# Optimization experiments

Measured on AMD Instinct MI355X. Metric: run time of the kernel, lower is better.

Reference implementation:

```python
import jax, jax.numpy as jnp
import numpy as np


def setup_inputs() -> dict:
    key = jax.random.key(0)
    k1, k2 = jax.random.split(key)
    B, D, H, W = 32, 256, 32, 32
    K = 1024
    z = jax.random.normal(k1, (B, D, H, W), dtype=jnp.float32)
    # torch init is uniform(-1/K, 1/K); randn scaled keeps same scale class
    embedding_weight = jax.random.uniform(k2, (K, D), dtype=jnp.float32,
                                          minval=-1.0 / K, maxval=1.0 / K)
    return {"z": z, "embedding_weight": embedding_weight}


def reference(z, embedding_weight):
    # z: [B, D, H, W] -> [B, H, W, D]
    z_nhwc = jnp.transpose(z, (0, 2, 3, 1))
    B, H, W, D = z_nhwc.shape
    z_flat = z_nhwc.reshape(-1, D)                      # [N, D]
    # squared distances: ||z||^2 + ||e||^2 - 2 z @ e^T   -> [N, K]
    d = (jnp.sum(z_flat ** 2, axis=1, keepdims=True)
         + jnp.sum(embedding_weight ** 2, axis=1)
         - 2.0 * z_flat @ embedding_weight.T)
    min_encoding_indices = jnp.argmin(d, axis=1)        # [N] int
    z_q = embedding_weight[min_encoding_indices].reshape(B, H, W, D)
    memodecode_loss = (jax.lax.stop_gradient(z_q) - z_nhwc) ** 2  # [B,H,W,D]
    z_q_out = jnp.transpose(z_q, (0, 3, 1, 2))          # [B, D, H, W]
    return (z_q_out, min_encoding_indices, memodecode_loss)
```

## Files before the change

### kernel.cpp

```cpp
#include <hip/hip_runtime.h>

#define DD 256
#define HWN 1024
#define NN 32768
#define KK 1024
#define MARGIN 1e-4f
#define FLAGBIT (1 << 30)

#define ZQ_OFF   0
#define IDX_OFF  8388608
#define LOSS_OFF 8421376

#define WS_NEED 38146112

typedef __attribute__((ext_vector_type(8))) _Float16 f16x8;
typedef __attribute__((ext_vector_type(4))) float f32x4;

__device__ __forceinline__ ushort f2h(float x) {
    _Float16 h = (_Float16)x;
    return *reinterpret_cast<ushort*>(&h);
}
__device__ __forceinline__ float h2f(ushort u) {
    _Float16 h = *reinterpret_cast<_Float16*>(&u);
    return (float)h;
}

__device__ __forceinline__ int swz(int r, int kgi) {
    return (r << 2) + (kgi ^ (r & 3) ^ ((r >> 2) & 3));
}

__global__ __launch_bounds__(64) void k_e2(const float* __restrict__ E,
                                           float* __restrict__ e2) {
    int k = (blockIdx.x << 6) + threadIdx.x;
    const float* row = E + (size_t)k * DD;
    float half_[2];
#pragma unroll
    for (int h = 0; h < 2; ++h) {
        const float* a = row + (h << 7);
        float r[8];
#pragma unroll
        for (int j = 0; j < 8; ++j) r[j] = __fmul_rn(a[j], a[j]);
        for (int i = 8; i < 128; i += 8) {
#pragma unroll
            for (int j = 0; j < 8; ++j) {
                float x = a[i + j];
                r[j] = __fadd_rn(r[j], __fmul_rn(x, x));
            }
        }
        half_[h] = __fadd_rn(__fadd_rn(__fadd_rn(r[0], r[1]), __fadd_rn(r[2], r[3])),
                             __fadd_rn(__fadd_rn(r[4], r[5]), __fadd_rn(r[6], r[7])));
    }
    e2[k] = __fadd_rn(half_[0], half_[1]);
}

__global__ __launch_bounds__(256) void k_prepZ2(const float* __restrict__ Z,
                                                ushort* __restrict__ Zh,
                                                float* __restrict__ z2) {
    __shared__ float zc[32][257];
    const int g = blockIdx.x;
    const int b = g >> 5;
    const int hw0 = (g & 31) << 5;
    const int th = threadIdx.x;
    const int n0 = (b << 10) + hw0;

#pragma unroll
    for (int j = 0; j < 32; ++j) {
        int li = (j << 8) + th;
        int d = li >> 5;
        int hl = li & 31;
        zc[hl][d] = Z[(size_t)((b << 8) + d) * HWN + hw0 + hl];
    }
    __syncthreads();

    {
        int r = th >> 3, c = th & 7;
        ushort hs[32];
#pragma unroll
        for (int i = 0; i < 32; ++i) hs[i] = f2h(zc[r][(c << 5) + i]);
        size_t addr = (size_t)(n0 + r) * DD + (c << 5);
#pragma unroll
        for (int q = 0; q < 4; ++q)
            *reinterpret_cast<f16x8*>(&Zh[addr + (q << 3)]) =
                *reinterpret_cast<f16x8*>(&hs[q << 3]);
    }

    {
        const int row = th >> 3, j = th & 7;
        const float* a = &zc[row][0];
        float x0 = a[j];
        float r0 = __fmul_rn(x0, x0);
        float x1 = a[128 + j];
        float r1 = __fmul_rn(x1, x1);
#pragma unroll
        for (int i = 8; i < 128; i += 8) {
            float y0 = a[i + j];
            r0 = __fadd_rn(r0, __fmul_rn(y0, y0));
            float y1 = a[128 + i + j];
            r1 = __fadd_rn(r1, __fmul_rn(y1, y1));
        }
#pragma unroll
        for (int m = 1; m <= 4; m <<= 1) {
            r0 = __fadd_rn(r0, __shfl_xor(r0, m));
            r1 = __fadd_rn(r1, __shfl_xor(r1, m));
        }
        if (j == 0) z2[n0 + row] = __fadd_rn(r0, r1);
    }
}

__global__ __launch_bounds__(256) void k_z2(const float* __restrict__ Z,
                                            float* __restrict__ z2) {
    int n = (blockIdx.x << 8) + threadIdx.x;
    int b = n >> 10, hw = n & 1023;
    const float* base = Z + (size_t)(b << 8) * HWN + hw;
    float half_[2];
#pragma unroll
    for (int h = 0; h < 2; ++h) {
        const float* a = base + (size_t)(h << 7) * HWN;
        float r[8];
#pragma unroll
        for (int j = 0; j < 8; ++j) {
            float x = a[(size_t)j * HWN];
            r[j] = __fmul_rn(x, x);
        }
        for (int i = 8; i < 128; i += 8) {
#pragma unroll
            for (int j = 0; j < 8; ++j) {
                float x = a[(size_t)(i + j) * HWN];
                r[j] = __fadd_rn(r[j], __fmul_rn(x, x));
            }
        }
        half_[h] = __fadd_rn(__fadd_rn(__fadd_rn(r[0], r[1]), __fadd_rn(r[2], r[3])),
                             __fadd_rn(__fadd_rn(r[4], r[5]), __fadd_rn(r[6], r[7])));
    }
    z2[n] = __fadd_rn(half_[0], half_[1]);
}

__global__ __launch_bounds__(256) void k_prepE(const float* __restrict__ E,
                                               ushort* __restrict__ Eh,
                                               int* __restrict__ flagCount) {
    if (blockIdx.x == 0 && threadIdx.x == 0) *flagCount = 0;
    int i4 = (blockIdx.x << 8) + threadIdx.x;
    float4 v = *reinterpret_cast<const float4*>(&E[(size_t)i4 << 2]);
    v.x *= 1024.f; v.y *= 1024.f; v.z *= 1024.f; v.w *= 1024.f;
    ushort4 h;
    h.x = f2h(v.x); h.y = f2h(v.y); h.z = f2h(v.z); h.w = f2h(v.w);
    *reinterpret_cast<ushort4*>(&Eh[(size_t)i4 << 2]) = h;
}

__device__ __forceinline__ void stage_kc(const ushort* __restrict__ Zh,
                                         const ushort* __restrict__ Eh,
                                         ushort* ldsbuf, int n0, int c0, int kc,
                                         int wid, int lane) {
#pragma unroll
    for (int is = 0; is < 4; ++is) {
        const int chunk = (wid << 2) + is;
        const int arr = chunk >> 3;
        const int cb8 = chunk & 7;
        const int s = (cb8 << 6) + lane;
        const int r = s >> 2;
        const int kgi = (s & 3) ^ (r & 3) ^ ((r >> 2) & 3);
        const ushort* g = (arr == 0) ? Zh + (size_t)(n0 + r) * DD
                                     : Eh + (size_t)(c0 + r) * DD;
        g += (kc << 5) + (kgi << 3);
        ushort* l = ldsbuf + arr * 4096 + (cb8 << 9);
        __builtin_amdgcn_global_load_lds(
            (const __attribute__((address_space(1))) void*)g,
            (__attribute__((address_space(3))) void*)l, 16, 0, 0);
    }
}

__global__ __launch_bounds__(256) void k_dist_mfma(const ushort* __restrict__ Zh,
                                                   const ushort* __restrict__ Eh,
                                                   const float* __restrict__ e2,
                                                   float* __restrict__ part) {
    __shared__ ushort lds[2][2][4096];
    float (*red)[2][3] = reinterpret_cast<float (*)[2][3]>(&lds[0][0][0]);

    const int B = blockIdx.x;
    const int xcd = B & 7;
    const int j = B >> 3;
    const int cb = j & 7;
    const int rb = (xcd << 5) + (j >> 3);
    const int n0 = rb << 7, c0 = cb << 7;
    const int th = threadIdx.x;
    const int wid = th >> 6, lane = th & 63;
    const int wr = wid >> 1, wc = wid & 1;
    const int fr = lane & 15, kgi = lane >> 4;

    f32x4 acc[4][4];
#pragma unroll
    for (int i = 0; i < 4; ++i)
#pragma unroll
        for (int jj = 0; jj < 4; ++jj) acc[i][jj] = (f32x4){0.f, 0.f, 0.f, 0.f};

    int zoff[4], eoff[4];
#pragma unroll
    for (int mi = 0; mi < 4; ++mi)
        zoff[mi] = swz((wr << 6) + (mi << 4) + fr, kgi) << 4;
#pragma unroll
    for (int ni = 0; ni < 4; ++ni)
        eoff[ni] = swz((wc << 6) + (ni << 4) + fr, kgi) << 4;

    stage_kc(Zh, Eh, &lds[0][0][0], n0, c0, 0, wid, lane);

    for (int kc = 0; kc < 8; ++kc) {
        __builtin_amdgcn_s_barrier();
        if (kc < 7) {
            stage_kc(Zh, Eh, &lds[(kc + 1) & 1][0][0], n0, c0, kc + 1, wid, lane);
            asm volatile("s_waitcnt vmcnt(4)" ::: "memory");
        } else {
            asm volatile("s_waitcnt vmcnt(0)" ::: "memory");
        }
        __builtin_amdgcn_s_barrier();

        const char* zb  = (const char*)&lds[kc & 1][0][0];
        const char* ebh = (const char*)&lds[kc & 1][1][0];
        f16x8 za[4], ea[4];
#pragma unroll
        for (int mi = 0; mi < 4; ++mi)
            za[mi] = *reinterpret_cast<const f16x8*>(zb + zoff[mi]);
#pragma unroll
        for (int ni = 0; ni < 4; ++ni)
            ea[ni] = *reinterpret_cast<const f16x8*>(ebh + eoff[ni]);
        __builtin_amdgcn_s_setprio(1);
#pragma unroll
        for (int mi = 0; mi < 4; ++mi)
#pragma unroll
            for (int ni = 0; ni < 4; ++ni)
                acc[mi][ni] = __builtin_amdgcn_mfma_f32_16x16x32_f16(za[mi], ea[ni], acc[mi][ni], 0, 0, 0);
        __builtin_amdgcn_s_setprio(0);
    }

    __syncthreads();

    float e2v[4];
#pragma unroll
    for (int ni = 0; ni < 4; ++ni) e2v[ni] = e2[c0 + (wc << 6) + (ni << 4) + fr];

#pragma unroll
    for (int mi = 0; mi < 4; ++mi) {
#pragma unroll
        for (int jj = 0; jj < 4; ++jj) {
            float m1 = __builtin_inff(), m2 = __builtin_inff(), bi = 3.4e38f;
#pragma unroll
            for (int ni = 0; ni < 4; ++ni) {
                float s = fmaf(-0x1p-9f, acc[mi][ni][jj], e2v[ni]);
                float c = (float)(c0 + (wc << 6) + (ni << 4) + fr);
                if (s < m1)      { m2 = m1; m1 = s; bi = c; }
                else if (s < m2) { m2 = s; }
            }
#pragma unroll
            for (int m = 1; m <= 8; m <<= 1) {
                float om1 = __shfl_xor(m1, m);
                float om2 = __shfl_xor(m2, m);
                float obi = __shfl_xor(bi, m);
                if (om1 < m1)       { m2 = fminf(m1, om2); m1 = om1; bi = obi; }
                else if (om1 == m1) { bi = fminf(bi, obi); m2 = m1; }
                else                { m2 = fminf(m2, om1); }
            }
            if (fr == 0) {
                int row = (wr << 6) + (mi << 4) + (kgi << 2) + jj;
                red[row][wc][0] = m1; red[row][wc][1] = m2; red[row][wc][2] = bi;
            }
        }
    }
    __syncthreads();
    if (th < 128) {
        float M1 = red[th][0][0], M2 = red[th][0][1], I = red[th][0][2];
        float v1 = red[th][1][0], v2 = red[th][1][1], vi = red[th][1][2];
        if (v1 < M1)       { M2 = fminf(M1, v2); M1 = v1; I = vi; }
        else if (v1 == M1) { I = fminf(I, vi); M2 = M1; }
        else               { M2 = fminf(M2, v1); }
        size_t p = ((size_t)(n0 + th) * 8 + cb) * 3;
        part[p] = M1; part[p + 1] = M2; part[p + 2] = I;
    }
}

__global__ __launch_bounds__(256) void k_combine(const float* __restrict__ part,
                                                 int* __restrict__ bestIdx,
                                                 int* __restrict__ flagList,
                                                 int* __restrict__ flagCount) {
    int n = (blockIdx.x << 8) + threadIdx.x;
    const float* p = part + (size_t)n * 24;
    float M1 = __builtin_inff(), M2 = __builtin_inff(), I = 3.4e38f;
    for (int c = 0; c < 8; ++c) {
        float v1 = p[c * 3], v2 = p[c * 3 + 1], vi = p[c * 3 + 2];
        if (v1 < M1)       { M2 = fminf(M1, v2); M1 = v1; I = vi; }
        else if (v1 == M1) { I = fminf(I, vi); M2 = M1; }
        else               { M2 = fminf(M2, v1); }
    }
    bestIdx[n] = (int)I;
    if (M2 - M1 < MARGIN) {
        int pos = atomicAdd(flagCount, 1);
        flagList[pos] = n;
    }
}

__global__ __launch_bounds__(256) void k_refine3(const float* __restrict__ Z,
                                                 const float* __restrict__ E,
                                                 const float* __restrict__ e2,
                                                 const float* __restrict__ z2,
                                                 int* __restrict__ bestIdx,
                                                 const int* __restrict__ flagList,
                                                 const int* __restrict__ flagCount) {
    __shared__ float zsh[DD];
    __shared__ float gbv[16];
    __shared__ int gbi[16];
    const int th = threadIdx.x;
    const int g = th >> 4;
    const int l = th & 15;
    const int cnt = *flagCount;

    for (int i = blockIdx.x; i < cnt; i += (int)gridDim.x) {
        const int n = flagList[i];
        const int b = n >> 10, hw = n & 1023;
        __syncthreads();
        if (th < DD) zsh[th] = Z[(size_t)((b << 8) + th) * HWN + hw];
        __syncthreads();
        float zr[16];
#pragma unroll
        for (int jq = 0; jq < 16; ++jq) zr[jq] = zsh[(l << 4) + jq];
        const float z2v = z2[n];
        float gbest = __builtin_inff();
        int bi = 0;

        for (int it = 0; it < 16; ++it) {
            double dots[4];
#pragma unroll
            for (int u = 0; u < 4; ++u) {
                const int c = (it << 6) + (u << 4) + g;
                const float* er = &E[(size_t)c * DD + (l << 4)];
                float4 a0 = *reinterpret_cast<const float4*>(er);
                float4 a1 = *reinterpret_cast<const float4*>(er + 4);
                float4 a2 = *reinterpret_cast<const float4*>(er + 8);
                float4 a3 = *reinterpret_cast<const float4*>(er + 12);
                double s0 = (double)a0.x * zr[0]  + (double)a0.y * zr[1]
                          + (double)a0.z * zr[2]  + (double)a0.w * zr[3];
                double s1 = (double)a1.x * zr[4]  + (double)a1.y * zr[5]
                          + (double)a1.z * zr[6]  + (double)a1.w * zr[7];
                double s2 = (double)a2.x * zr[8]  + (double)a2.y * zr[9]
                          + (double)a2.z * zr[10] + (double)a2.w * zr[11];
                double s3 = (double)a3.x * zr[12] + (double)a3.y * zr[13]
                          + (double)a3.z * zr[14] + (double)a3.w * zr[15];
                dots[u] = (s0 + s1) + (s2 + s3);
            }
#pragma unroll
            for (int m = 1; m <= 8; m <<= 1) {
#pragma unroll
                for (int u = 0; u < 4; ++u)
                    dots[u] += __shfl_xor(dots[u], m);
            }
            if (l == 0) {
#pragma unroll
                for (int u = 0; u < 4; ++u) {
                    const int c = (it << 6) + (u << 4) + g;
                    float cc = (float)dots[u];
                    float t2 = __fmul_rn(2.0f, cc);
                    float gg = __fsub_rn(__fadd_rn(z2v, e2[c]), t2);
                    if (gg < gbest) { gbest = gg; bi = c; }
                }
            }
        }
        if (l == 0) { gbv[g] = gbest; gbi[g] = bi; }
        __syncthreads();
        if (th == 0) {
            float best = gbv[0]; int bbi = gbi[0];
            for (int q = 1; q < 16; ++q) {
                float v = gbv[q]; int vi = gbi[q];
                if (v < best || (v == best && vi < bbi)) { best = v; bbi = vi; }
            }
            bestIdx[n] = bbi;
        }
    }
}

#define UPD(m1, m2, i1, s, k)                            \
    do {                                                 \
        if ((s) < (m1)) { m2 = m1; m1 = (s); i1 = (k); } \
        else if ((s) < (m2)) { m2 = (s); }               \
    } while (0)

#define FMAJ(j, EV, C)                                   \
    acc[0][j] = fmaf(z4.x, EV.C, acc[0][j]);             \
    acc[1][j] = fmaf(z4.y, EV.C, acc[1][j]);             \
    acc[2][j] = fmaf(z4.z, EV.C, acc[2][j]);             \
    acc[3][j] = fmaf(z4.w, EV.C, acc[3][j]);

#define UROUND(u, C)                                                          \
    {                                                                         \
        float4 z4 = *reinterpret_cast<const float4*>(&zs[dq + u][ty4]);       \
        FMAJ(0, e0, C) FMAJ(1, e1, C) FMAJ(2, e2v, C) FMAJ(3, e3, C)          \
        FMAJ(4, e4, C) FMAJ(5, e5, C) FMAJ(6, e6, C) FMAJ(7, e7, C)           \
    }

__global__ __launch_bounds__(256, 3) void k_dist_f32(const float* __restrict__ Z,
                                                     const float* __restrict__ E,
                                                     const float* __restrict__ e2,
                                                     int* __restrict__ bestIdx) {
    __shared__ float zs[64][68];
    __shared__ float es[128][68];
    const int th = threadIdx.x;
    const int n0 = blockIdx.x << 6;
    const int b = n0 >> 10;
    const int hw0 = n0 & 1023;
    const int tx = th & 15;
    const int ty = th >> 4;
    const int ty4 = ty << 2;
    float m1[4], m2[4];
    int idx[4];
#pragma unroll
    for (int i = 0; i < 4; ++i) { m1[i] = __builtin_inff(); m2[i] = __builtin_inff(); idx[i] = 0; }
    for (int ct = 0; ct < 8; ++ct) {
        float acc[4][8];
#pragma unroll
        for (int i = 0; i < 4; ++i)
#pragma unroll
            for (int j = 0; j < 8; ++j) acc[i][j] = 0.f;
        for (int dc = 0; dc < 4; ++dc) {
            __syncthreads();
#pragma unroll
            for (int j = 0; j < 4; ++j) {
                int i4 = (j << 8) + th;
                int dd = i4 >> 4;
                int rr = (i4 & 15) << 2;
                *reinterpret_cast<float4*>(&zs[dd][rr]) =
                    *reinterpret_cast<const float4*>(
                        &Z[(size_t)((b << 8) + (dc << 6) + dd) * HWN + hw0 + rr]);
            }
#pragma unroll
            for (int j = 0; j < 8; ++j) {
                int i4 = (j << 8) + th;
                int c = i4 >> 4;
                int d4 = (i4 & 15) << 2;
                *reinterpret_cast<float4*>(&es[c][d4]) =
                    *reinterpret_cast<const float4*>(
                        &E[(size_t)((ct << 7) + c) * DD + (dc << 6) + d4]);
            }
            __syncthreads();
#pragma unroll
            for (int dq = 0; dq < 64; dq += 4) {
                float4 e0 = *reinterpret_cast<const float4*>(&es[tx][dq]);
                float4 e1 = *reinterpret_cast<const float4*>(&es[tx + 16][dq]);
                float4 e2v = *reinterpret_cast<const float4*>(&es[tx + 32][dq]);
                float4 e3 = *reinterpret_cast<const float4*>(&es[tx + 48][dq]);
                float4 e4 = *reinterpret_cast<const float4*>(&es[tx + 64][dq]);
                float4 e5 = *reinterpret_cast<const float4*>(&es[tx + 80][dq]);
                float4 e6 = *reinterpret_cast<const float4*>(&es[tx + 96][dq]);
                float4 e7 = *reinterpret_cast<const float4*>(&es[tx + 112][dq]);
                UROUND(0, x)
                UROUND(1, y)
                UROUND(2, z)
                UROUND(3, w)
            }
        }
#pragma unroll
        for (int j = 0; j < 8; ++j) {
            int c = (ct << 7) + tx + (j << 4);
            float en = e2[c];
#pragma unroll
            for (int i = 0; i < 4; ++i) {
                float s = fmaf(-2.f, acc[i][j], en);
                UPD(m1[i], m2[i], idx[i], s, c);
            }
        }
    }
    __syncthreads();
    float* red = &es[0][0];
#pragma unroll
    for (int i = 0; i < 4; ++i) {
        int r = ty4 + i;
        int base = ((r << 4) + tx) * 3;
        red[base] = m1[i]; red[base + 1] = m2[i]; red[base + 2] = (float)idx[i];
    }
    __syncthreads();
    if (th < 64) {
        float M1 = __builtin_inff(), M2 = __builtin_inff(), I = 3.4e38f;
        for (int t = 0; t < 16; ++t) {
            int base = ((th << 4) + t) * 3;
            float v1 = red[base], v2 = red[base + 1], vi = red[base + 2];
            if (v1 < M1)       { M2 = fminf(M1, v2); M1 = v1; I = vi; }
            else if (v1 == M1) { I = fminf(I, vi); M2 = fminf(M2, v1); M2 = fminf(M2, v2); }
            else               { M2 = fminf(M2, v1); }
        }
        int id = (int)I;
        bestIdx[n0 + th] = (M2 - M1 < MARGIN) ? (id | FLAGBIT) : id;
    }
}

__global__ __launch_bounds__(64) void k_refine(const float* __restrict__ Z,
                                               const float* __restrict__ E,
                                               const float* __restrict__ e2,
                                               const float* __restrict__ z2,
                                               int* __restrict__ bestIdx) {
    __shared__ float zr[DD];
    const int l = threadIdx.x;
    for (int i = 0; i < 16; ++i) {
        int n = (blockIdx.x << 4) + i;
        if (!(bestIdx[n] & FLAGBIT)) continue;
        int b = n >> 10, hw = n & 1023;
        __syncthreads();
#pragma unroll
        for (int j = 0; j < 4; ++j)
            zr[(l << 2) + j] = Z[(size_t)((b << 8) + (l << 2) + j) * HWN + hw];
        __syncthreads();
        const float z2v = z2[n];
        float gbest = __builtin_inff();
        int bi = KK;
        for (int kk = 0; kk < 16; ++kk) {
            int k = (kk << 6) + l;
            double dot = 0.0;
            for (int d = 0; d < DD; d += 4) {
                float4 e4 = *reinterpret_cast<const float4*>(&E[(size_t)k * DD + d]);
                dot += (double)e4.x * zr[d]     + (double)e4.y * zr[d + 1]
                     + (double)e4.z * zr[d + 2] + (double)e4.w * zr[d + 3];
            }
            float c = (float)dot;
            float t = __fmul_rn(2.0f, c);
            float gg = __fsub_rn(__fadd_rn(z2v, e2[k]), t);
            if (gg < gbest) { gbest = gg; bi = k; }
        }
#pragma unroll
        for (int off = 32; off > 0; off >>= 1) {
            float og = __shfl_down(gbest, off);
            int oi = __shfl_down(bi, off);
            if (og < gbest || (og == gbest && oi < bi)) { gbest = og; bi = oi; }
        }
        if (l == 0) bestIdx[n] = bi;
    }
}

__global__ __launch_bounds__(256) void k_out(const ushort* __restrict__ Zh,
                                             const float* __restrict__ E,
                                             const int* __restrict__ bestIdx,
                                             float* __restrict__ out) {
    __shared__ int idxs[64];
    const int th = threadIdx.x;
    const int n0 = blockIdx.x << 6;
    const int b = n0 >> 10;
    const int hw0 = n0 & 1023;

    if (th < 64) {
        int id = bestIdx[n0 + th] & 1023;
        idxs[th] = id;
        out[IDX_OFF + n0 + th] = (float)id;
    }
    __syncthreads();

#pragma unroll
    for (int j = 0; j < 16; ++j) {
        int i4 = (j << 8) + th;
        int r = i4 >> 6;
        int f = (i4 & 63) << 2;
        int n = n0 + r;
        float4 e4 = *reinterpret_cast<const float4*>(&E[(size_t)idxs[r] * DD + f]);
        ushort4 zu = *reinterpret_cast<const ushort4*>(&Zh[(size_t)n * DD + f]);
        float4 o;
        float t;
        t = e4.x - h2f(zu.x); o.x = t * t;
        t = e4.y - h2f(zu.y); o.y = t * t;
        t = e4.z - h2f(zu.z); o.z = t * t;
        t = e4.w - h2f(zu.w); o.w = t * t;
        *reinterpret_cast<float4*>(&out[LOSS_OFF + (size_t)n * DD + f]) = o;
    }

#pragma unroll
    for (int dc = 0; dc < 4; ++dc)
#pragma unroll
        for (int j = 0; j < 16; ++j) {
            int li = (j << 8) + th;
            int dd = li >> 6;
            int r = li & 63;
            out[ZQ_OFF + (size_t)((b << 8) + (dc << 6) + dd) * HWN + hw0 + r] =
                E[(size_t)idxs[r] * DD + (dc << 6) + dd];
        }
}

__global__ __launch_bounds__(256) void k_out_f32(const float* __restrict__ Z,
                                                 const float* __restrict__ E,
                                                 const int* __restrict__ bestIdx,
                                                 float* __restrict__ out) {
    __shared__ float zc[64][68];
    __shared__ int idxs[64];
    const int th = threadIdx.x;
    const int n0 = blockIdx.x << 6;
    const int b = n0 >> 10;
    const int hw0 = n0 & 1023;

    if (th < 64) {
        int id = bestIdx[n0 + th] & 1023;
        idxs[th] = id;
        out[IDX_OFF + n0 + th] = (float)id;
    }
    __syncthreads();

    for (int dc = 0; dc < 4; ++dc) {
        __syncthreads();
#pragma unroll
        for (int j = 0; j < 16; ++j) {
            int li = (j << 8) + th;
            int dd = li >> 6;
            int r = li & 63;
            zc[r][dd] = Z[(size_t)((b << 8) + (dc << 6) + dd) * HWN + hw0 + r];
        }
        __syncthreads();
#pragma unroll
        for (int j = 0; j < 4; ++j) {
            int i4 = (j << 8) + th;
            int r = i4 >> 4;
            int f = (i4 & 15) << 2;
            float4 e4 = *reinterpret_cast<const float4*>(
                &E[(size_t)idxs[r] * DD + (dc << 6) + f]);
            float4 z4 = *reinterpret_cast<const float4*>(&zc[r][f]);
            float4 o;
            o.x = (e4.x - z4.x) * (e4.x - z4.x);
            o.y = (e4.y - z4.y) * (e4.y - z4.y);
            o.z = (e4.z - z4.z) * (e4.z - z4.z);
            o.w = (e4.w - z4.w) * (e4.w - z4.w);
            *reinterpret_cast<float4*>(
                &out[LOSS_OFF + (size_t)(n0 + r) * DD + (dc << 6) + f]) = o;
        }
#pragma unroll
        for (int j = 0; j < 16; ++j) {
            int li = (j << 8) + th;
            int dd = li >> 6;
            int r = li & 63;
            out[ZQ_OFF + (size_t)((b << 8) + (dc << 6) + dd) * HWN + hw0 + r] =
                E[(size_t)idxs[r] * DD + (dc << 6) + dd];
        }
    }
}

extern "C" void kernel_launch(void* const* d_in, const int* in_sizes, int n_in,
                              void* d_out, int out_size, void* d_ws, size_t ws_size,
                              hipStream_t stream) {
    const float* Z = (const float*)d_in[0];
    const float* E = (const float*)d_in[1];
    float* out = (float*)d_out;
    char* ws = (char*)d_ws;
    float* e2 = (float*)ws;
    float* z2 = (float*)(ws + 4096);
    int* bestIdx = (int*)(ws + 135168);

    k_e2<<<KK / 64, 64, 0, stream>>>(E, e2);

    if (ws_size >= WS_NEED) {
        float* part = (float*)(ws + 266240);
        ushort* Eh = (ushort*)(ws + 3411968);
        ushort* Zh = (ushort*)(ws + 4460544);
        int* flagCount = (int*)(ws + 38014976);
        int* flagList = (int*)(ws + 38015040);
        k_prepE<<<256, 256, 0, stream>>>(E, Eh, flagCount);
        k_prepZ2<<<1024, 256, 0, stream>>>(Z, Zh, z2);
        k_dist_mfma<<<2048, 256, 0, stream>>>(Zh, Eh, e2, part);
        k_combine<<<NN / 256, 256, 0, stream>>>(part, bestIdx, flagList, flagCount);
        k_refine3<<<2048, 256, 0, stream>>>(Z, E, e2, z2, bestIdx, flagList, flagCount);
        k_out<<<NN / 64, 256, 0, stream>>>(Zh, E, bestIdx, out);
    } else {
        k_z2<<<NN / 256, 256, 0, stream>>>(Z, z2);
        k_dist_f32<<<NN / 64, 256, 0, stream>>>(Z, E, e2, bestIdx);
        k_refine<<<NN / 16, 64, 0, stream>>>(Z, E, e2, z2, bestIdx);
        k_out_f32<<<NN / 64, 256, 0, stream>>>(Z, E, bestIdx, out);
    }
}
```

Before: 156.9 us.

## Split refine work per flagged row into four codebook quarters with atomic min merge

The exact-precision refine pass now splits each ambiguous row's 1024-code search into four blocks of 256 codes each. Each block packs its (distance, index) result into a 64-bit value, and the blocks merge through atomicMin on a per-row slot. A new small kernel then writes the winning indices back. This raises parallelism when few rows are flagged, at the cost of an extra launch, reloading z per quarter, and 64-bit atomics. Because distances can be negative, packing float bits as unsigned may order them wrongly.

```diff
diff --git a/kernel.cpp b/kernel.cpp
--- a/kernel.cpp
+++ b/kernel.cpp
@@ -15,6 +15,7 @@
 
 typedef __attribute__((ext_vector_type(8))) _Float16 f16x8;
 typedef __attribute__((ext_vector_type(4))) float f32x4;
+typedef unsigned long long u64;
 
 __device__ __forceinline__ ushort f2h(float x) {
     _Float16 h = (_Float16)x;
@@ -279,7 +280,8 @@
 __global__ __launch_bounds__(256) void k_combine(const float* __restrict__ part,
                                                  int* __restrict__ bestIdx,
                                                  int* __restrict__ flagList,
-                                                 int* __restrict__ flagCount) {
+                                                 int* __restrict__ flagCount,
+                                                 u64* __restrict__ bestG) {
     int n = (blockIdx.x << 8) + threadIdx.x;
     const float* p = part + (size_t)n * 24;
     float M1 = __builtin_inff(), M2 = __builtin_inff(), I = 3.4e38f;
@@ -291,28 +293,30 @@
     }
     bestIdx[n] = (int)I;
     if (M2 - M1 < MARGIN) {
+        bestG[n] = ~0ull;
         int pos = atomicAdd(flagCount, 1);
         flagList[pos] = n;
     }
 }
 
-__global__ __launch_bounds__(256) void k_refine3(const float* __restrict__ Z,
+__global__ __launch_bounds__(256) void k_refine4(const float* __restrict__ Z,
                                                  const float* __restrict__ E,
                                                  const float* __restrict__ e2,
                                                  const float* __restrict__ z2,
-                                                 int* __restrict__ bestIdx,
                                                  const int* __restrict__ flagList,
-                                                 const int* __restrict__ flagCount) {
+                                                 const int* __restrict__ flagCount,
+                                                 u64* __restrict__ bestG) {
     __shared__ float zsh[DD];
     __shared__ float gbv[16];
     __shared__ int gbi[16];
     const int th = threadIdx.x;
     const int g = th >> 4;
     const int l = th & 15;
-    const int cnt = *flagCount;
-
-    for (int i = blockIdx.x; i < cnt; i += (int)gridDim.x) {
-        const int n = flagList[i];
+    const int cnt4 = (*flagCount) << 2;
+
+    for (int jj = blockIdx.x; jj < cnt4; jj += (int)gridDim.x) {
+        const int n = flagList[jj >> 2];
+        const int q = jj & 3;
         const int b = n >> 10, hw = n & 1023;
         __syncthreads();
         if (th < DD) zsh[th] = Z[(size_t)((b << 8) + th) * HWN + hw];
@@ -324,11 +328,12 @@
         float gbest = __builtin_inff();
         int bi = 0;
 
-        for (int it = 0; it < 16; ++it) {
+        const int base = q << 8;
+        for (int it = 0; it < 4; ++it) {
             double dots[4];
 #pragma unroll
             for (int u = 0; u < 4; ++u) {
-                const int c = (it << 6) + (u << 4) + g;
+                const int c = base + (it << 6) + (u << 4) + g;
                 const float* er = &E[(size_t)c * DD + (l << 4)];
                 float4 a0 = *reinterpret_cast<const float4*>(er);
                 float4 a1 = *reinterpret_cast<const float4*>(er + 4);
@@ -353,7 +358,7 @@
             if (l == 0) {
 #pragma unroll
                 for (int u = 0; u < 4; ++u) {
-                    const int c = (it << 6) + (u << 4) + g;
+                    const int c = base + (it << 6) + (u << 4) + g;
                     float cc = (float)dots[u];
                     float t2 = __fmul_rn(2.0f, cc);
                     float gg = __fsub_rn(__fadd_rn(z2v, e2[c]), t2);
@@ -365,12 +370,24 @@
         __syncthreads();
         if (th == 0) {
             float best = gbv[0]; int bbi = gbi[0];
-            for (int q = 1; q < 16; ++q) {
-                float v = gbv[q]; int vi = gbi[q];
+            for (int qq = 1; qq < 16; ++qq) {
+                float v = gbv[qq]; int vi = gbi[qq];
                 if (v < best || (v == best && vi < bbi)) { best = v; bbi = vi; }
             }
-            bestIdx[n] = bbi;
-        }
+            u64 pack = ((u64)__float_as_uint(best) << 32) | (unsigned)bbi;
+            atomicMin(&bestG[n], pack);
+        }
+    }
+}
+
+__global__ __launch_bounds__(256) void k_final(const int* __restrict__ flagList,
+                                               const int* __restrict__ flagCount,
+                                               const u64* __restrict__ bestG,
+                                               int* __restrict__ bestIdx) {
+    const int cnt = *flagCount;
+    for (int j = (blockIdx.x << 8) + threadIdx.x; j < cnt; j += (int)(gridDim.x << 8)) {
+        int n = flagList[j];
+        bestIdx[n] = (int)(unsigned)(bestG[n] & 0xFFFFFFFFull);
     }
 }
 
@@ -647,13 +664,15 @@
         float* part = (float*)(ws + 266240);
         ushort* Eh = (ushort*)(ws + 3411968);
         ushort* Zh = (ushort*)(ws + 4460544);
+        u64* bestG = (u64*)(ws + 21237760);
         int* flagCount = (int*)(ws + 38014976);
         int* flagList = (int*)(ws + 38015040);
         k_prepE<<<256, 256, 0, stream>>>(E, Eh, flagCount);
         k_prepZ2<<<1024, 256, 0, stream>>>(Z, Zh, z2);
         k_dist_mfma<<<2048, 256, 0, stream>>>(Zh, Eh, e2, part);
-        k_combine<<<NN / 256, 256, 0, stream>>>(part, bestIdx, flagList, flagCount);
-        k_refine3<<<2048, 256, 0, stream>>>(Z, E, e2, z2, bestIdx, flagList, flagCount);
+        k_combine<<<NN / 256, 256, 0, stream>>>(part, bestIdx, flagList, flagCount, bestG);
+        k_refine4<<<4096, 256, 0, stream>>>(Z, E, e2, z2, flagList, flagCount, bestG);
+        k_final<<<64, 256, 0, stream>>>(flagList, flagCount, bestG, bestIdx);
         k_out<<<NN / 64, 256, 0, stream>>>(Zh, E, bestIdx, out);
     } else {
         k_z2<<<NN / 256, 256, 0, stream>>>(Z, z2);
```

Result: no change. 158.5 us (+1.1%).
